# Kernel optimization log

Measured on AMD Instinct MI355X. Metric: run time of the kernel, lower is better.

Reference implementation:

```python
import jax, jax.numpy as jnp
import numpy as np

B, K, F, E = 32, 1024, 128, 128  # batch, window_size(num_nodes), n_features, embed_dim
OUT2 = 125                       # lin2 output dim (hardcoded in module)
ALPHA = 0.2                      # LeakyReLU negative slope


def setup_inputs() -> dict:
    key = jax.random.key(0)
    ks = jax.random.split(key, 7)
    x = jax.random.normal(ks[0], (B, K, F), dtype=jnp.float32)
    lin_w = jax.random.normal(ks[1], (E, F), dtype=jnp.float32) * 0.05
    lin_b = jax.random.normal(ks[2], (E,), dtype=jnp.float32) * 0.01
    a = jax.random.normal(ks[3], (2 * E, 1), dtype=jnp.float32) * 0.1  # xavier-ish
    bias = jax.random.normal(ks[4], (K, K), dtype=jnp.float32) * 0.02
    lin2_w = jax.random.normal(ks[5], (OUT2, K), dtype=jnp.float32) * 0.03
    lin2_b = jax.random.normal(ks[6], (OUT2,), dtype=jnp.float32) * 0.01
    return {"x": x, "lin_w": lin_w, "lin_b": lin_b, "a": a, "bias": bias,
            "lin2_w": lin2_w, "lin2_b": lin2_b}


def reference(x, lin_w, lin_b, a, bias, lin2_w, lin2_b):
    # Wx = lin(x): [B,K,E]
    Wx = jnp.einsum('bkf,ef->bke', x, lin_w) + lin_b
    # Additive attention scores. Original concatenates (Wx_i, Wx_j) -> [B,K,K,2E]
    # then matmuls with a [2E,1]. Identity: concat @ a == Wx_i@a1 + Wx_j@a2.
    a1 = a[:E, 0]   # [E]
    a2 = a[E:, 0]   # [E]
    s1 = Wx @ a1    # [B,K]  (row/query term, from repeat_interleave)
    s2 = Wx @ a2    # [B,K]  (col/key term, from repeat)
    e = jax.nn.leaky_relu(s1[:, :, None] + s2[:, None, :], negative_slope=ALPHA)
    e = e + bias                              # [B,K,K]
    attention = jax.nn.softmax(e, axis=2)     # softmax over last dim (keys)
    h = jnp.einsum('bij,bjf->bif', attention, x) + x   # [B,K,F], residual
    # permute(0,2,1) -> [B,F,K]; lin2 contracts K -> 125
    h2 = jnp.einsum('bkf,ok->bfo', h, lin2_w) + lin2_b  # [B,F,125]
    h2 = jax.nn.relu(h2)
    return (h2, attention)
```

## Files before the change

### kernel.cpp

```cpp
#include <hip/hip_runtime.h>

#define B_ 32
#define K_ 1024
#define F_ 128
#define E_ 128
#define OUT2_ 125
#define ALPHA_ 0.2f

typedef __bf16 bf16x8_t __attribute__((ext_vector_type(8)));
typedef float  f32x4_t  __attribute__((ext_vector_type(4)));

__device__ __forceinline__ unsigned short f2bf(float f) {
    unsigned u = __float_as_uint(f);
    u = (u + 0x7fffu + ((u >> 16) & 1u)) >> 16;
    return (unsigned short)u;
}

__global__ void k_prep(const float* __restrict__ lin_w, const float* __restrict__ lin_b,
                       const float* __restrict__ a, float* __restrict__ ws) {
    int t = threadIdx.x;
    if (t < 128) {
        float acc = 0.f;
        for (int e = 0; e < E_; ++e) acc += lin_w[e * F_ + t] * a[e];
        ws[t] = acc;
    } else {
        int f = t - 128;
        float acc = 0.f;
        for (int e = 0; e < E_; ++e) acc += lin_w[e * F_ + f] * a[E_ + e];
        ws[128 + f] = acc;
    }
    if (t == 0) { float c = 0.f; for (int e = 0; e < E_; ++e) c += lin_b[e] * a[e];       ws[256] = c; }
    if (t == 1) { float c = 0.f; for (int e = 0; e < E_; ++e) c += lin_b[e] * a[E_ + e];  ws[257] = c; }
}

__global__ __launch_bounds__(256) void k_scores(const float* __restrict__ x,
                                                const float* __restrict__ ws,
                                                float* __restrict__ s1, float* __restrict__ s2) {
    int wave = threadIdx.x >> 6;
    int lane = threadIdx.x & 63;
    int row = blockIdx.x * 4 + wave;
    const float* xr = x + (size_t)row * F_;
    float x0 = xr[lane], x1 = xr[lane + 64];
    float p1 = x0 * ws[lane]       + x1 * ws[lane + 64];
    float p2 = x0 * ws[128 + lane] + x1 * ws[192 + lane];
    for (int m = 32; m; m >>= 1) { p1 += __shfl_xor(p1, m, 64); p2 += __shfl_xor(p2, m, 64); }
    if (lane == 0) { s1[row] = p1 + ws[256]; s2[row] = p2 + ws[257]; }
}

__global__ __launch_bounds__(256) void k_xt(const float* __restrict__ x,
                                            unsigned short* __restrict__ xt) {
    int kt = blockIdx.x;
    int b  = blockIdx.y;
    int t  = threadIdx.x;
    __shared__ float xs[64 * 132];
    const float* xb = x + ((size_t)b * K_ + kt * 64) * F_;
#pragma unroll
    for (int q = 0; q < 8; ++q) {
        int flat = q * 256 + t;
        int kk = flat >> 5, f4 = flat & 31;
        float4 v = *(const float4*)(xb + (size_t)kk * F_ + f4 * 4);
        xs[kk * 132 + f4 * 4]     = v.x;
        xs[kk * 132 + f4 * 4 + 1] = v.y;
        xs[kk * 132 + f4 * 4 + 2] = v.z;
        xs[kk * 132 + f4 * 4 + 3] = v.w;
    }
    __syncthreads();
    int f = t >> 1, half = t & 1;
    union { unsigned short u[32]; uint4 v[4]; } pack;
#pragma unroll
    for (int i = 0; i < 32; ++i) pack.u[i] = f2bf(xs[(half * 32 + i) * 132 + f]);
    unsigned short* dst = xt + (((size_t)(b * 16 + kt) * 128 + f) * 64 + half * 32);
    uint4* d4 = (uint4*)dst;
#pragma unroll
    for (int i = 0; i < 4; ++i) d4[i] = pack.v[i];
}

__global__ __launch_bounds__(256) void k_softmax(const float* __restrict__ s1,
                                                 const float* __restrict__ s2,
                                                 const float* __restrict__ bias,
                                                 float* __restrict__ att) {
    int i = blockIdx.x >> 5;
    int b = blockIdx.x & 31;
    int t = threadIdx.x;
    float sv = s1[b * K_ + i];
    float4 s2v = ((const float4*)(s2 + b * K_))[t];
    float4 bv  = ((const float4*)(bias + (size_t)i * K_))[t];
    float e[4];
    {
        float v;
        v = sv + s2v.x; v = v > 0.f ? v : ALPHA_ * v; e[0] = __expf(v + bv.x);
        v = sv + s2v.y; v = v > 0.f ? v : ALPHA_ * v; e[1] = __expf(v + bv.y);
        v = sv + s2v.z; v = v > 0.f ? v : ALPHA_ * v; e[2] = __expf(v + bv.z);
        v = sv + s2v.w; v = v > 0.f ? v : ALPHA_ * v; e[3] = __expf(v + bv.w);
    }
    float sum = e[0] + e[1] + e[2] + e[3];
    for (int m = 32; m; m >>= 1) sum += __shfl_xor(sum, m, 64);
    __shared__ float reds[4];
    int wave = t >> 6, lane = t & 63;
    if (lane == 0) reds[wave] = sum;
    __syncthreads();
    sum = reds[0] + reds[1] + reds[2] + reds[3];
    float r = 1.f / sum;
    float4 o; o.x = e[0] * r; o.y = e[1] * r; o.z = e[2] * r; o.w = e[3] * r;
    ((float4*)(att + ((size_t)b * K_ + i) * K_))[t] = o;
}

__global__ __launch_bounds__(256) void k_attx(const float* __restrict__ att,
                                              const unsigned short* __restrict__ xt,
                                              const float* __restrict__ x,
                                              unsigned short* __restrict__ ht) {
    int b  = blockIdx.y;
    int i0 = blockIdx.x * 32;
    int t  = threadIdx.x;
    int wave = t >> 6, lane = t & 63;
    int quad = lane >> 4, l15 = lane & 15;

    __shared__ unsigned short A_s[32 * 72];
    __shared__ unsigned short X_s[128 * 72];

    const float* ab = att + ((size_t)b * K_ + i0) * K_;

    f32x4_t acc[2][2];
#pragma unroll
    for (int m = 0; m < 2; ++m)
#pragma unroll
        for (int n = 0; n < 2; ++n) acc[m][n] = (f32x4_t)(0.f);

    int ai = t >> 3, aq = t & 7;
    int xf = t >> 1, xh = t & 1;

    for (int kt = 0; kt < 16; ++kt) {
        int k0 = kt * 64;
        __syncthreads();
        {
            const float* src = ab + (size_t)ai * K_ + k0 + aq * 8;
            float4 v0 = *(const float4*)(src);
            float4 v1 = *(const float4*)(src + 4);
            union { unsigned short u[8]; uint4 v; } p;
            p.u[0] = f2bf(v0.x); p.u[1] = f2bf(v0.y); p.u[2] = f2bf(v0.z); p.u[3] = f2bf(v0.w);
            p.u[4] = f2bf(v1.x); p.u[5] = f2bf(v1.y); p.u[6] = f2bf(v1.z); p.u[7] = f2bf(v1.w);
            *(uint4*)&A_s[ai * 72 + aq * 8] = p.v;
        }
        {
            const uint4* src = (const uint4*)(xt + ((size_t)(b * 16 + kt)) * 128 * 64) + t * 4;
            uint4* d = (uint4*)&X_s[xf * 72 + xh * 32];
#pragma unroll
            for (int q = 0; q < 4; ++q) d[q] = src[q];
        }
        __syncthreads();
#pragma unroll
        for (int kh = 0; kh < 2; ++kh) {
            bf16x8_t af[2], bff[2];
#pragma unroll
            for (int m = 0; m < 2; ++m)
                af[m] = *(const bf16x8_t*)&A_s[(m * 16 + l15) * 72 + kh * 32 + quad * 8];
#pragma unroll
            for (int n = 0; n < 2; ++n)
                bff[n] = *(const bf16x8_t*)&X_s[(wave * 32 + n * 16 + l15) * 72 + kh * 32 + quad * 8];
#pragma unroll
            for (int m = 0; m < 2; ++m)
#pragma unroll
                for (int n = 0; n < 2; ++n)
                    acc[m][n] = __builtin_amdgcn_mfma_f32_16x16x32_bf16(af[m], bff[n], acc[m][n], 0, 0, 0);
        }
    }
#pragma unroll
    for (int m = 0; m < 2; ++m) {
#pragma unroll
        for (int n = 0; n < 2; ++n) {
            int f = wave * 32 + n * 16 + l15;
            int ib = i0 + m * 16 + quad * 4;
            union { unsigned short u[4]; ushort4 v; } p;
#pragma unroll
            for (int r = 0; r < 4; ++r) {
                int i = ib + r;
                p.u[r] = f2bf(acc[m][n][r] + x[((size_t)b * K_ + i) * F_ + f]);
            }
            *(ushort4*)&ht[((size_t)b * F_ + f) * K_ + ib] = p.v;
        }
    }
}

__global__ __launch_bounds__(256) void k_out2m(const unsigned short* __restrict__ ht,
                                               const float* __restrict__ w2,
                                               const float* __restrict__ b2,
                                               float* __restrict__ out) {
    int b  = blockIdx.y;
    int f0 = blockIdx.x * 64;
    int t  = threadIdx.x;
    int wave = t >> 6, lane = t & 63;
    int quad = lane >> 4, l15 = lane & 15;

    __shared__ unsigned short W_s[128 * 72];
    __shared__ unsigned short H_s[64 * 72];

    f32x4_t acc[8];
#pragma unroll
    for (int m = 0; m < 8; ++m) acc[m] = (f32x4_t)(0.f);

    int wo = t >> 1, wq = t & 1;
    int hf = t >> 2, hq = t & 3;

    for (int kt = 0; kt < 16; ++kt) {
        int k0 = kt * 64;
        __syncthreads();
        {
            union { unsigned short u[32]; uint4 v[4]; } p;
            if (wo < OUT2_) {
                const float* src = w2 + (size_t)wo * K_ + k0 + wq * 32;
#pragma unroll
                for (int q = 0; q < 8; ++q) {
                    float4 v = *(const float4*)(src + q * 4);
                    p.u[q * 4]     = f2bf(v.x);
                    p.u[q * 4 + 1] = f2bf(v.y);
                    p.u[q * 4 + 2] = f2bf(v.z);
                    p.u[q * 4 + 3] = f2bf(v.w);
                }
            } else {
#pragma unroll
                for (int q = 0; q < 4; ++q) p.v[q] = make_uint4(0, 0, 0, 0);
            }
            uint4* d = (uint4*)&W_s[wo * 72 + wq * 32];
#pragma unroll
            for (int q = 0; q < 4; ++q) d[q] = p.v[q];
        }
        {
            const uint4* src = (const uint4*)(ht + ((size_t)b * F_ + f0 + hf) * K_ + k0) + hq * 2;
            uint4* d = (uint4*)&H_s[hf * 72 + hq * 16];
            d[0] = src[0]; d[1] = src[1];
        }
        __syncthreads();
#pragma unroll
        for (int kh = 0; kh < 2; ++kh) {
            bf16x8_t bf = *(const bf16x8_t*)&H_s[(wave * 16 + l15) * 72 + kh * 32 + quad * 8];
#pragma unroll
            for (int m = 0; m < 8; ++m) {
                bf16x8_t af = *(const bf16x8_t*)&W_s[(m * 16 + l15) * 72 + kh * 32 + quad * 8];
                acc[m] = __builtin_amdgcn_mfma_f32_16x16x32_bf16(af, bf, acc[m], 0, 0, 0);
            }
        }
    }
    int f = f0 + wave * 16 + l15;
    float* orow = out + ((size_t)b * F_ + f) * OUT2_;
#pragma unroll
    for (int m = 0; m < 8; ++m) {
        int ob = m * 16 + quad * 4;
#pragma unroll
        for (int r = 0; r < 4; ++r) {
            int o = ob + r;
            if (o < OUT2_) {
                float v = acc[m][r] + b2[o];
                orow[o] = v > 0.f ? v : 0.f;
            }
        }
    }
}

extern "C" void kernel_launch(void* const* d_in, const int* in_sizes, int n_in,
                              void* d_out, int out_size, void* d_ws, size_t ws_size,
                              hipStream_t stream) {
    const float* x      = (const float*)d_in[0];
    const float* lin_w  = (const float*)d_in[1];
    const float* lin_b  = (const float*)d_in[2];
    const float* a      = (const float*)d_in[3];
    const float* bias   = (const float*)d_in[4];
    const float* lin2_w = (const float*)d_in[5];
    const float* lin2_b = (const float*)d_in[6];

    float* out = (float*)d_out;
    float* h2  = out;
    float* att = out + (size_t)B_ * F_ * OUT2_;

    float* ws = (float*)d_ws;
    float* s1 = ws + 512;
    float* s2 = ws + 512 + B_ * K_;
    unsigned short* ht = (unsigned short*)(ws + 512 + 2 * B_ * K_);
    unsigned short* xt = ht + (size_t)B_ * K_ * F_;

    k_prep<<<1, 256, 0, stream>>>(lin_w, lin_b, a, ws);
    k_scores<<<(B_ * K_) / 4, 256, 0, stream>>>(x, ws, s1, s2);
    k_xt<<<dim3(16, B_), 256, 0, stream>>>(x, xt);
    k_softmax<<<B_ * K_, 256, 0, stream>>>(s1, s2, bias, att);
    k_attx<<<dim3(K_ / 32, B_), 256, 0, stream>>>(att, xt, x, ht);
    k_out2m<<<dim3(2, B_), 256, 0, stream>>>(ht, lin2_w, lin2_b, h2);
}
```

Baseline: 293.8 us.

## Double-buffer xt tiles in attx, load attention directly to registers, split-K lin2

In k_attx, attention values are now read straight from global memory into registers and converted to bf16 there, so the A shared-memory staging is gone. The xt tiles are double-buffered in shared memory with an XOR swizzle, and the next tile is prefetched during the MFMAs, which leaves one barrier per iteration. k_out2m, which launched only 64 blocks, is split four ways along K into partial sums kept in the reused xt workspace, and a new epilogue kernel adds bias and applies ReLU. This trades an extra launch and partial-sum traffic for more parallelism, and the direct attention loads are less coalesced than before.

```diff
diff --git a/kernel.cpp b/kernel.cpp
--- a/kernel.cpp
+++ b/kernel.cpp
@@ -105,20 +105,20 @@
     ((float4*)(att + ((size_t)b * K_ + i) * K_))[t] = o;
 }
 
-__global__ __launch_bounds__(256) void k_attx(const float* __restrict__ att,
-                                              const unsigned short* __restrict__ xt,
-                                              const float* __restrict__ x,
-                                              unsigned short* __restrict__ ht) {
+__global__ __launch_bounds__(256, 4) void k_attx(const float* __restrict__ att,
+                                                 const unsigned short* __restrict__ xt,
+                                                 const float* __restrict__ x,
+                                                 unsigned short* __restrict__ ht) {
     int b  = blockIdx.y;
     int i0 = blockIdx.x * 32;
     int t  = threadIdx.x;
     int wave = t >> 6, lane = t & 63;
     int quad = lane >> 4, l15 = lane & 15;
 
-    __shared__ unsigned short A_s[32 * 72];
-    __shared__ unsigned short X_s[128 * 72];
-
-    const float* ab = att + ((size_t)b * K_ + i0) * K_;
+    __shared__ unsigned short X_s[2][128 * 64];
+
+    const float* ab  = att + ((size_t)b * K_ + i0) * K_;
+    const uint4* xtb = (const uint4*)(xt + (size_t)b * 16 * 128 * 64);
 
     f32x4_t acc[2][2];
 #pragma unroll
@@ -126,43 +126,65 @@
 #pragma unroll
         for (int n = 0; n < 2; ++n) acc[m][n] = (f32x4_t)(0.f);
 
-    int ai = t >> 3, aq = t & 7;
-    int xf = t >> 1, xh = t & 1;
-
+#pragma unroll
+    for (int q = 0; q < 4; ++q) {
+        int flat = q * 256 + t;
+        int row = flat >> 3, g = flat & 7;
+        *(uint4*)&X_s[0][row * 64 + 8 * (g ^ (row & 7))] = xtb[flat];
+    }
+    __syncthreads();
+
+    int cur = 0;
     for (int kt = 0; kt < 16; ++kt) {
         int k0 = kt * 64;
-        __syncthreads();
-        {
-            const float* src = ab + (size_t)ai * K_ + k0 + aq * 8;
-            float4 v0 = *(const float4*)(src);
-            float4 v1 = *(const float4*)(src + 4);
-            union { unsigned short u[8]; uint4 v; } p;
-            p.u[0] = f2bf(v0.x); p.u[1] = f2bf(v0.y); p.u[2] = f2bf(v0.z); p.u[3] = f2bf(v0.w);
-            p.u[4] = f2bf(v1.x); p.u[5] = f2bf(v1.y); p.u[6] = f2bf(v1.z); p.u[7] = f2bf(v1.w);
-            *(uint4*)&A_s[ai * 72 + aq * 8] = p.v;
-        }
-        {
-            const uint4* src = (const uint4*)(xt + ((size_t)(b * 16 + kt)) * 128 * 64) + t * 4;
-            uint4* d = (uint4*)&X_s[xf * 72 + xh * 32];
-#pragma unroll
-            for (int q = 0; q < 4; ++q) d[q] = src[q];
-        }
-        __syncthreads();
+        uint4 xn[4];
+        if (kt < 15) {
+            const uint4* src = xtb + (size_t)(kt + 1) * 1024;
+#pragma unroll
+            for (int q = 0; q < 4; ++q) xn[q] = src[q * 256 + t];
+        }
+        float4 av[2][2][2];
+#pragma unroll
+        for (int m = 0; m < 2; ++m) {
+            const float* arow = ab + (size_t)(m * 16 + l15) * K_ + k0 + quad * 8;
+#pragma unroll
+            for (int kh = 0; kh < 2; ++kh) {
+                av[m][kh][0] = *(const float4*)(arow + kh * 32);
+                av[m][kh][1] = *(const float4*)(arow + kh * 32 + 4);
+            }
+        }
 #pragma unroll
         for (int kh = 0; kh < 2; ++kh) {
             bf16x8_t af[2], bff[2];
 #pragma unroll
-            for (int m = 0; m < 2; ++m)
-                af[m] = *(const bf16x8_t*)&A_s[(m * 16 + l15) * 72 + kh * 32 + quad * 8];
-#pragma unroll
-            for (int n = 0; n < 2; ++n)
-                bff[n] = *(const bf16x8_t*)&X_s[(wave * 32 + n * 16 + l15) * 72 + kh * 32 + quad * 8];
+            for (int m = 0; m < 2; ++m) {
+                union { unsigned short u[8]; bf16x8_t v; } p;
+                float4 v0 = av[m][kh][0], v1 = av[m][kh][1];
+                p.u[0] = f2bf(v0.x); p.u[1] = f2bf(v0.y); p.u[2] = f2bf(v0.z); p.u[3] = f2bf(v0.w);
+                p.u[4] = f2bf(v1.x); p.u[5] = f2bf(v1.y); p.u[6] = f2bf(v1.z); p.u[7] = f2bf(v1.w);
+                af[m] = p.v;
+            }
+#pragma unroll
+            for (int n = 0; n < 2; ++n) {
+                int row = wave * 32 + n * 16 + l15;
+                bff[n] = *(const bf16x8_t*)&X_s[cur][row * 64 + 8 * (((kh << 2) | quad) ^ (row & 7))];
+            }
 #pragma unroll
             for (int m = 0; m < 2; ++m)
 #pragma unroll
                 for (int n = 0; n < 2; ++n)
                     acc[m][n] = __builtin_amdgcn_mfma_f32_16x16x32_bf16(af[m], bff[n], acc[m][n], 0, 0, 0);
         }
+        if (kt < 15) {
+#pragma unroll
+            for (int q = 0; q < 4; ++q) {
+                int flat = q * 256 + t;
+                int row = flat >> 3, g = flat & 7;
+                *(uint4*)&X_s[cur ^ 1][row * 64 + 8 * (g ^ (row & 7))] = xn[q];
+            }
+        }
+        __syncthreads();
+        cur ^= 1;
     }
 #pragma unroll
     for (int m = 0; m < 2; ++m) {
@@ -183,10 +205,10 @@
 
 __global__ __launch_bounds__(256) void k_out2m(const unsigned short* __restrict__ ht,
                                                const float* __restrict__ w2,
-                                               const float* __restrict__ b2,
-                                               float* __restrict__ out) {
+                                               float* __restrict__ part) {
     int b  = blockIdx.y;
     int f0 = blockIdx.x * 64;
+    int ks = blockIdx.z;
     int t  = threadIdx.x;
     int wave = t >> 6, lane = t & 63;
     int quad = lane >> 4, l15 = lane & 15;
@@ -201,7 +223,8 @@
     int wo = t >> 1, wq = t & 1;
     int hf = t >> 2, hq = t & 3;
 
-    for (int kt = 0; kt < 16; ++kt) {
+    int kt0 = ks * 4;
+    for (int kt = kt0; kt < kt0 + 4; ++kt) {
         int k0 = kt * 64;
         __syncthreads();
         {
@@ -241,19 +264,23 @@
         }
     }
     int f = f0 + wave * 16 + l15;
-    float* orow = out + ((size_t)b * F_ + f) * OUT2_;
-#pragma unroll
-    for (int m = 0; m < 8; ++m) {
-        int ob = m * 16 + quad * 4;
-#pragma unroll
-        for (int r = 0; r < 4; ++r) {
-            int o = ob + r;
-            if (o < OUT2_) {
-                float v = acc[m][r] + b2[o];
-                orow[o] = v > 0.f ? v : 0.f;
-            }
-        }
-    }
+    float* prow = part + ((size_t)(ks * 32 + b) * 128 + f) * 128;
+#pragma unroll
+    for (int m = 0; m < 8; ++m)
+        *(f32x4_t*)&prow[m * 16 + quad * 4] = acc[m];
+}
+
+__global__ __launch_bounds__(256) void k_out2e(const float* __restrict__ part,
+                                               const float* __restrict__ b2,
+                                               float* __restrict__ out) {
+    int idx = blockIdx.x * 256 + threadIdx.x;
+    if (idx >= B_ * F_ * OUT2_) return;
+    int o  = idx % OUT2_;
+    int bf = idx / OUT2_;
+    float v = b2[o];
+#pragma unroll
+    for (int s = 0; s < 4; ++s) v += part[((size_t)s * 4096 + bf) * 128 + o];
+    out[idx] = v > 0.f ? v : 0.f;
 }
 
 extern "C" void kernel_launch(void* const* d_in, const int* in_sizes, int n_in,
@@ -276,11 +303,13 @@
     float* s2 = ws + 512 + B_ * K_;
     unsigned short* ht = (unsigned short*)(ws + 512 + 2 * B_ * K_);
     unsigned short* xt = ht + (size_t)B_ * K_ * F_;
+    float* part = (float*)xt;
 
     k_prep<<<1, 256, 0, stream>>>(lin_w, lin_b, a, ws);
     k_scores<<<(B_ * K_) / 4, 256, 0, stream>>>(x, ws, s1, s2);
     k_xt<<<dim3(16, B_), 256, 0, stream>>>(x, xt);
     k_softmax<<<B_ * K_, 256, 0, stream>>>(s1, s2, bias, att);
     k_attx<<<dim3(K_ / 32, B_), 256, 0, stream>>>(att, xt, x, ht);
-    k_out2m<<<dim3(2, B_), 256, 0, stream>>>(ht, lin2_w, lin2_b, h2);
-}
+    k_out2m<<<dim3(2, B_, 4), 256, 0, stream>>>(ht, lin2_w, part);
+    k_out2e<<<(B_ * F_ * OUT2_ + 255) / 256, 256, 0, stream>>>(part, lin2_b, h2);
+}
```

Measured after the change: 287.6 us. -2.1%, faster.
